# Kernel optimization log

Hardware: AMD Instinct MI355X
Metric: run time of the kernel (lower is better)

Reference implementation:

```python
import jax, jax.numpy as jnp
import numpy as np

N = 50000      # nodes
E = 800000     # edges (avg degree 16)
D = 128        # extended_lat_size = latent_size(124) + 4
G = 256        # number of graphs in the batch
H = 8 * D      # 1024, hidden width of MLP stack


def _w(k, shape):
    return jax.random.normal(k, shape, jnp.float32) * 0.02


def setup_inputs() -> dict:
    key = jax.random.key(0)
    ks = jax.random.split(key, 20)
    x = jax.random.normal(ks[0], (N, D), jnp.float32)
    edge_index = jax.random.randint(ks[1], (2, E), 0, N, dtype=jnp.int32)
    batch_vector = jnp.sort(jax.random.randint(ks[2], (N,), 0, G, dtype=jnp.int32))
    return {
        "x": x,
        "edge_index": edge_index,
        "batch_vector": batch_vector,
        # GCNConv layers
        "W1": _w(ks[3], (D, 2 * D)), "b1": jnp.zeros((2 * D,), jnp.float32),
        "W2": _w(ks[4], (2 * D, D)), "b2": jnp.zeros((D,), jnp.float32),
        # lazy Linear stack (in-dims resolved from dataflow)
        "Wl1": _w(ks[5], (D, D)),   "bl1": jnp.zeros((D,), jnp.float32),
        "Wl2": _w(ks[6], (D, H)),   "bl2": jnp.zeros((H,), jnp.float32),
        "Wl22": _w(ks[7], (H, H)),  "bl22": jnp.zeros((H,), jnp.float32),
        "Wl23": _w(ks[8], (H, H)),  "bl23": jnp.zeros((H,), jnp.float32),
        "Wl3": _w(ks[9], (H, D)),   "bl3": jnp.zeros((D,), jnp.float32),
    }


def gcn_conv(x, W, b, row, col):
    """PyG GCNConv: linear transform, add self-loops, symmetric norm, scatter-add."""
    h = x @ W  # [N, F_out]
    n = x.shape[0]
    loop = jnp.arange(n, dtype=row.dtype)
    r = jnp.concatenate([row, loop])   # source nodes
    c = jnp.concatenate([col, loop])   # target nodes
    deg = jax.ops.segment_sum(jnp.ones_like(c, dtype=h.dtype), c, num_segments=n)
    dinv = jnp.where(deg > 0, jax.lax.rsqrt(deg), 0.0)
    norm = dinv[r] * dinv[c]                         # [E+N]
    msg = h[r] * norm[:, None]                       # gather + scale
    out = jax.ops.segment_sum(msg, c, num_segments=n)  # scatter-add
    return out + b


def global_mean_pool(x, batch, num_graphs):
    s = jax.ops.segment_sum(x, batch, num_segments=num_graphs)
    cnt = jax.ops.segment_sum(jnp.ones((x.shape[0],), x.dtype), batch, num_segments=num_graphs)
    return s / jnp.maximum(cnt, 1.0)[:, None]


def reference(x, edge_index, batch_vector, W1, b1, W2, b2,
              Wl1, bl1, Wl2, bl2, Wl22, bl22, Wl23, bl23, Wl3, bl3):
    row, col = edge_index[0], edge_index[1]
    h = jax.nn.relu(gcn_conv(x, W1, b1, row, col))
    h = jax.nn.relu(gcn_conv(h, W2, b2, row, col))
    g = global_mean_pool(h, batch_vector, G)         # [G, D]
    g = jax.nn.relu(g @ Wl1 + bl1)
    g = jax.nn.relu(g @ Wl2 + bl2)
    g = jax.nn.relu(g @ Wl22 + bl22)
    g = jax.nn.relu(g @ Wl23 + bl23)
    g = g @ Wl3 + bl3                                 # [G, D]
    return jnp.squeeze(g).reshape(-1)                 # flatten -> [G*D]
```

## Files before the change

kernel.cpp:

```cpp
#include <hip/hip_runtime.h>


typedef __attribute__((ext_vector_type(8))) short bf16x8;
typedef __attribute__((ext_vector_type(8))) ushort u16x8;
typedef __attribute__((ext_vector_type(4))) float f32x4;

#define ADJ_STRIDE 64

__device__ __forceinline__ ushort f2bf(float f) {
    unsigned u = __float_as_uint(f);
    unsigned r = (u + 0x7FFFu + ((u >> 16) & 1u)) >> 16;
    return (ushort)r;
}
__device__ __forceinline__ float bf2f(ushort h) {
    return __uint_as_float(((unsigned)h) << 16);
}
__device__ __forceinline__ float bflo(unsigned u) {
    return __uint_as_float(u << 16);
}
__device__ __forceinline__ float bfhi(unsigned u) {
    return __uint_as_float(u & 0xffff0000u);
}
__device__ __forceinline__ float idinv(int d) {
    return rsqrtf((float)(d + 1));
}
__device__ __forceinline__ void gload16(const ushort* g, ushort* l) {
    __builtin_amdgcn_global_load_lds(
        (const __attribute__((address_space(1))) void*)g,
        (__attribute__((address_space(3))) void*)l, 16, 0, 0);
}

#define SWZ(r) (((r) >> 1) & 3)

struct PreArgs {
    const int* row;
    const int* col;
    int E, N;
    int* indeg;
    int* adjf;
    const float* W[7];
    ushort* Th[7];
    ushort* Tl[7];
    int K[7], Nn[7], off[8];
    const float* x;
    ushort* xb;
    int total8;
    int nFill, nT;
};

__global__ __launch_bounds__(256) void preproc_mega_kernel(PreArgs a) {
    __shared__ float sm[64][65];
    int bid = blockIdx.x;
    int tid = threadIdx.x;

    if (bid < a.nFill) {
        int r = bid & 7, chunk = bid >> 3;
        int lo = (int)(((long long)a.N * r) >> 3);
        int hi = (int)(((long long)a.N * (r + 1)) >> 3);
        int E4 = a.E >> 2;
#pragma unroll
        for (int v = 0; v < 2; ++v) {
            int i = chunk * 512 + v * 256 + tid;
            if (i < E4) {
                int c0 = __builtin_nontemporal_load(a.col + i * 4 + 0);
                int c1 = __builtin_nontemporal_load(a.col + i * 4 + 1);
                int c2 = __builtin_nontemporal_load(a.col + i * 4 + 2);
                int c3 = __builtin_nontemporal_load(a.col + i * 4 + 3);
                int r0 = __builtin_nontemporal_load(a.row + i * 4 + 0);
                int r1 = __builtin_nontemporal_load(a.row + i * 4 + 1);
                int r2 = __builtin_nontemporal_load(a.row + i * 4 + 2);
                int r3 = __builtin_nontemporal_load(a.row + i * 4 + 3);
                if (c0 >= lo && c0 < hi) {
                    int p = atomicAdd(&a.indeg[c0], 1);
                    if (p < ADJ_STRIDE) a.adjf[(c0 << 6) + p] = r0;
                }
                if (c1 >= lo && c1 < hi) {
                    int p = atomicAdd(&a.indeg[c1], 1);
                    if (p < ADJ_STRIDE) a.adjf[(c1 << 6) + p] = r1;
                }
                if (c2 >= lo && c2 < hi) {
                    int p = atomicAdd(&a.indeg[c2], 1);
                    if (p < ADJ_STRIDE) a.adjf[(c2 << 6) + p] = r2;
                }
                if (c3 >= lo && c3 < hi) {
                    int p = atomicAdd(&a.indeg[c3], 1);
                    if (p < ADJ_STRIDE) a.adjf[(c3 << 6) + p] = r3;
                }
            }
        }
        if (bid == 0 && tid < (a.E & 3)) {
            int e = (a.E & ~3) + tid;
            int c = a.col[e];
            int p = atomicAdd(&a.indeg[c], 1);
            if (p < ADJ_STRIDE) a.adjf[(c << 6) + p] = a.row[e];
        }
        return;
    }

    if (bid < a.nFill + a.nT) {
        int b = bid - a.nFill;
        int j = 0;
#pragma unroll
        for (int t = 1; t < 7; ++t) if (b >= a.off[t]) j = t;
        int local = b - a.off[j];
        int K = a.K[j], Nn = a.Nn[j];
        int kt = K >> 6;
        int k0 = (local % kt) * 64, n0 = (local / kt) * 64;
        const float* W = a.W[j];
        ushort* Th = a.Th[j];
        ushort* Tl = a.Tl[j];

        int r = tid >> 2, cq = tid & 3;
#pragma unroll
        for (int i = 0; i < 4; ++i) {
            float4 v = *(const float4*)(W + (size_t)(k0 + r) * Nn + n0 + cq * 16 + i * 4);
            sm[r][cq * 16 + i * 4 + 0] = v.x;
            sm[r][cq * 16 + i * 4 + 1] = v.y;
            sm[r][cq * 16 + i * 4 + 2] = v.z;
            sm[r][cq * 16 + i * 4 + 3] = v.w;
        }
        __syncthreads();
        int n = tid >> 2, kq = tid & 3;
        ushort h[16], l[16];
#pragma unroll
        for (int i = 0; i < 16; ++i) {
            float v = sm[kq * 16 + i][n];
            h[i] = f2bf(v);
            l[i] = f2bf(v - bf2f(h[i]));
        }
        size_t o = (size_t)(n0 + n) * K + k0 + kq * 16;
        *(u16x8*)(&Th[o]) = *(u16x8*)&h[0];
        *(u16x8*)(&Th[o + 8]) = *(u16x8*)&h[8];
        *(u16x8*)(&Tl[o]) = *(u16x8*)&l[0];
        *(u16x8*)(&Tl[o + 8]) = *(u16x8*)&l[8];
        return;
    }

    {
        int idx = (bid - a.nFill - a.nT) * 256 + tid;
        if (idx >= a.total8) return;
        const float4* xp = (const float4*)a.x;
        float4 v0 = xp[idx * 2], v1 = xp[idx * 2 + 1];
        ushort h[8] = {f2bf(v0.x), f2bf(v0.y), f2bf(v0.z), f2bf(v0.w),
                       f2bf(v1.x), f2bf(v1.y), f2bf(v1.z), f2bf(v1.w)};
        *(u16x8*)(a.xb + (size_t)idx * 8) = *(u16x8*)&h[0];
    }
}

template<int MODE>
__global__ void aggregate_bf16_kernel(const ushort* __restrict__ hsb,
                                      const int* __restrict__ indeg,
                                      const int* __restrict__ adjf,
                                      const float* __restrict__ bias,
                                      ushort* __restrict__ outh, ushort* __restrict__ outl,
                                      int N) {
    int wv = (blockIdx.x * blockDim.x + threadIdx.x) >> 6;
    int lane = threadIdx.x & 63;
    int half = lane >> 5, l32 = lane & 31;
    int node = wv * 2 + half;
    bool active = node < N;
    int nd = active ? node : N - 1;
    const uint2* base = (const uint2*)hsb;
    int degRaw = indeg[nd];
    float dself = idinv(degRaw);
    uint2 sa = base[(size_t)nd * 32 + l32];
    float sw = (MODE == 1) ? dself : 1.f;
    float ax = sw * bflo(sa.x), ay = sw * bfhi(sa.x);
    float az = sw * bflo(sa.y), aw = sw * bfhi(sa.y);
    int s = nd << 6;
    int deg = active ? min(degRaw, ADJ_STRIDE) : 0;
    int mx = max(deg, __shfl_xor(deg, 32));
    for (int j = 0; j < mx; j += 16) {
        int idx[16]; float wgt[16];
#pragma unroll
        for (int k = 0; k < 16; ++k) {
            int jj = j + k;
            bool valid = jj < deg;
            int ld = adjf[s + (valid ? jj : 0)];
            idx[k] = valid ? ld : 0;
            wgt[k] = valid ? 1.f : 0.f;
        }
        uint2 v[16];
#pragma unroll
        for (int k = 0; k < 16; ++k) v[k] = base[(size_t)idx[k] * 32 + l32];
        if (MODE == 1) {
#pragma unroll
            for (int k = 0; k < 16; ++k) wgt[k] *= idinv(indeg[idx[k]]);
        }
#pragma unroll
        for (int k = 0; k < 16; ++k) {
            ax = fmaf(wgt[k], bflo(v[k].x), ax);
            ay = fmaf(wgt[k], bfhi(v[k].x), ay);
            az = fmaf(wgt[k], bflo(v[k].y), az);
            aw = fmaf(wgt[k], bfhi(v[k].y), aw);
        }
    }
    if (!active) return;
    if (MODE == 0) {
        float4 b = ((const float4*)bias)[l32];
        ax = fmaxf(fmaf(ax, dself, b.x), 0.f);
        ay = fmaxf(fmaf(ay, dself, b.y), 0.f);
        az = fmaxf(fmaf(az, dself, b.z), 0.f);
        aw = fmaxf(fmaf(aw, dself, b.w), 0.f);
        ushort h0 = f2bf(ax), h1 = f2bf(ay), h2 = f2bf(az), h3 = f2bf(aw);
        uint2 hv = make_uint2((unsigned)h0 | ((unsigned)h1 << 16),
                              (unsigned)h2 | ((unsigned)h3 << 16));
        ((uint2*)outh)[(size_t)node * 32 + l32] = hv;
    } else {
        ax *= dself; ay *= dself; az *= dself; aw *= dself;
        ushort h0 = f2bf(ax), h1 = f2bf(ay), h2 = f2bf(az), h3 = f2bf(aw);
        uint2 hv = make_uint2((unsigned)h0 | ((unsigned)h1 << 16),
                              (unsigned)h2 | ((unsigned)h3 << 16));
        ushort l0 = f2bf(ax - bf2f(h0)), l1 = f2bf(ay - bf2f(h1));
        ushort l2 = f2bf(az - bf2f(h2)), l3 = f2bf(aw - bf2f(h3));
        uint2 lv = make_uint2((unsigned)l0 | ((unsigned)l1 << 16),
                              (unsigned)l2 | ((unsigned)l3 << 16));
        ((uint2*)outh)[(size_t)node * 32 + l32] = hv;
        ((uint2*)outl)[(size_t)node * 32 + l32] = lv;
    }
}

__global__ __launch_bounds__(512) void gcn_mid_kernel(
        const ushort* __restrict__ Ah, const ushort* __restrict__ Al,
        const ushort* __restrict__ B1h, const ushort* __restrict__ B1l,
        const ushort* __restrict__ B2h, const ushort* __restrict__ B2l,
        const float* __restrict__ bias1, const int* __restrict__ indeg,
        ushort* __restrict__ outb, int M) {
    __shared__ __align__(16) ushort t1f[2 * 128 * 256 + 2 * 128 * 32];
    const int tid = threadIdx.x;
    const int w = tid >> 6, lane = tid & 63;
    const int bm = blockIdx.x * 128;
    const int sq = lane >> 4, r16 = lane & 15;

    {
        const int wr = w >> 2, wc = w & 3;
        f32x4 acc1[4][4];
#pragma unroll
        for (int i = 0; i < 4; ++i)
#pragma unroll
            for (int j = 0; j < 4; ++j) acc1[i][j] = (f32x4)0.f;

        for (int kk = 0; kk < 128; kk += 32) {
            {
                int rowi = w * 16 + (lane >> 2);
                int u = lane & 3;
                int colk = kk + 8 * (u ^ SWZ(rowi));
                gload16(Ah + (size_t)(bm + rowi) * 128 + colk, t1f + w * 512);
                gload16(Al + (size_t)(bm + rowi) * 128 + colk, t1f + 4096 + w * 512);
            }
#pragma unroll
            for (int v = 0; v < 2; ++v) {
                int chunk = v * 8 + w;
                int rowi = chunk * 16 + (lane >> 2);
                int u = lane & 3;
                int colk = kk + 8 * (u ^ SWZ(rowi));
                gload16(B1h + (size_t)rowi * 128 + colk, t1f + 8192 + chunk * 512);
                gload16(B1l + (size_t)rowi * 128 + colk, t1f + 16384 + chunk * 512);
            }
            __syncthreads();

            bf16x8 ah[4], al[4], bh[4], bl[4];
#pragma unroll
            for (int f = 0; f < 4; ++f) {
                int ra = wr * 64 + f * 16 + r16;
                int oa = ra * 32 + 8 * (sq ^ SWZ(ra));
                ah[f] = *(const bf16x8*)(t1f + oa);
                al[f] = *(const bf16x8*)(t1f + 4096 + oa);
                int rb = wc * 64 + f * 16 + r16;
                int ob = rb * 32 + 8 * (sq ^ SWZ(rb));
                bh[f] = *(const bf16x8*)(t1f + 8192 + ob);
                bl[f] = *(const bf16x8*)(t1f + 16384 + ob);
            }
#pragma unroll
            for (int i = 0; i < 4; ++i)
#pragma unroll
                for (int j = 0; j < 4; ++j) {
                    acc1[i][j] = __builtin_amdgcn_mfma_f32_16x16x32_bf16(ah[i], bh[j], acc1[i][j], 0, 0, 0);
                    acc1[i][j] = __builtin_amdgcn_mfma_f32_16x16x32_bf16(ah[i], bl[j], acc1[i][j], 0, 0, 0);
                    acc1[i][j] = __builtin_amdgcn_mfma_f32_16x16x32_bf16(al[i], bh[j], acc1[i][j], 0, 0, 0);
                }
            __syncthreads();
        }

        const int q4 = lane >> 4;
#pragma unroll
        for (int j = 0; j < 4; ++j) {
            int col = wc * 64 + j * 16 + r16;
            float bv = bias1[col];
            int cslot = col >> 3, coff = col & 7;
#pragma unroll
            for (int i = 0; i < 4; ++i) {
                int rowb = wr * 64 + i * 16 + q4 * 4;
#pragma unroll
                for (int r = 0; r < 4; ++r) {
                    int rowt = rowb + r;
                    float v = fmaxf(acc1[i][j][r] + bv, 0.f);
                    ushort h = f2bf(v);
                    ushort lo = f2bf(v - bf2f(h));
                    int a = rowt * 256 + (((cslot ^ (rowt & 7)) << 3) + coff);
                    t1f[a] = h;
                    t1f[32768 + a] = lo;
                }
            }
        }
    }

    {
        const int wr2 = w >> 1, wc2 = w & 1;
        const int q4 = lane >> 4;
        f32x4 acc2[2][4];
#pragma unroll
        for (int i = 0; i < 2; ++i)
#pragma unroll
            for (int j = 0; j < 4; ++j) acc2[i][j] = (f32x4)0.f;

        for (int kk = 0; kk < 256; kk += 32) {
            {
                int rowi = w * 16 + (lane >> 2);
                int u = lane & 3;
                int colk = kk + 8 * (u ^ SWZ(rowi));
                gload16(B2h + (size_t)rowi * 256 + colk, t1f + 65536 + w * 512);
                gload16(B2l + (size_t)rowi * 256 + colk, t1f + 69632 + w * 512);
            }
            __syncthreads();

            bf16x8 a2h[2], a2l[2], b2h[4], b2l[4];
#pragma unroll
            for (int f = 0; f < 2; ++f) {
                int ra = wr2 * 32 + f * 16 + r16;
                int k0 = kk + sq * 8;
                int ao = ra * 256 + (((k0 >> 3) ^ (ra & 7)) << 3);
                a2h[f] = *(const bf16x8*)(t1f + ao);
                a2l[f] = *(const bf16x8*)(t1f + 32768 + ao);
            }
#pragma unroll
            for (int f = 0; f < 4; ++f) {
                int rb = wc2 * 64 + f * 16 + r16;
                int ob = rb * 32 + 8 * (sq ^ SWZ(rb));
                b2h[f] = *(const bf16x8*)(t1f + 65536 + ob);
                b2l[f] = *(const bf16x8*)(t1f + 69632 + ob);
            }
#pragma unroll
            for (int i = 0; i < 2; ++i)
#pragma unroll
                for (int j = 0; j < 4; ++j) {
                    acc2[i][j] = __builtin_amdgcn_mfma_f32_16x16x32_bf16(a2h[i], b2h[j], acc2[i][j], 0, 0, 0);
                    acc2[i][j] = __builtin_amdgcn_mfma_f32_16x16x32_bf16(a2h[i], b2l[j], acc2[i][j], 0, 0, 0);
                    acc2[i][j] = __builtin_amdgcn_mfma_f32_16x16x32_bf16(a2l[i], b2h[j], acc2[i][j], 0, 0, 0);
                }
            __syncthreads();
        }

#pragma unroll
        for (int i = 0; i < 2; ++i) {
            int row0 = bm + wr2 * 32 + i * 16 + q4 * 4;
            if (row0 >= M) continue;
#pragma unroll
            for (int j = 0; j < 4; ++j) {
                int col = wc2 * 64 + j * 16 + r16;
#pragma unroll
                for (int r = 0; r < 4; ++r) {
                    float dv = idinv(indeg[row0 + r]);
                    outb[(size_t)(row0 + r) * 128 + col] =
                        f2bf(acc2[i][j][r] * dv);
                }
            }
        }
    }
}

template<int BM, int BN, int EPI>
__global__ __launch_bounds__(256) void gemm_bf16x3_kernel(
        const ushort* __restrict__ Ah, const ushort* __restrict__ Al,
        const ushort* __restrict__ Bth, const ushort* __restrict__ Btl,
        const float* __restrict__ bias,
        float* __restrict__ Cf, ushort* __restrict__ Ch, ushort* __restrict__ Cl,
        int M, int N, int K, int kChunk) {
    constexpr int WMm = BM / 2, WMn = BN / 2;
    constexpr int FRm = WMm / 16, FRn = WMn / 16;
    __shared__ __align__(16) ushort lds[(2 * BM + 2 * BN) * 32];
    const int tbB[4] = {0, BM * 64, 2 * BM * 64, (2 * BM + BN) * 64};

    const int tid = threadIdx.x;
    const int w = tid >> 6, lane = tid & 63;
    const int wr = w >> 1, wc = w & 1;
    const int bm = blockIdx.x * BM, bn = blockIdx.y * BN;
    const int k0 = blockIdx.z * kChunk;
    int k1 = k0 + kChunk; if (k1 > K) k1 = K;

    const ushort* srcs[4] = {
        Ah  + (size_t)bm * K, Al  + (size_t)bm * K,
        Bth + (size_t)bn * K, Btl + (size_t)bn * K };

    f32x4 acc[FRm][FRn];
#pragma unroll
    for (int i = 0; i < FRm; ++i)
#pragma unroll
        for (int j = 0; j < FRn; ++j) acc[i][j] = (f32x4)0.f;

    const int sq = lane >> 4, r16 = lane & 15;

    for (int kk = k0; kk < k1; kk += 32) {
#pragma unroll
        for (int t = 0; t < 4; ++t) {
            const int rows = (t < 2) ? BM : BN;
            const int nv = rows / 64;
#pragma unroll
            for (int v = 0; v < nv; ++v) {
                int chunk = v * 4 + w;
                int rowi = chunk * 16 + (lane >> 2);
                int u = lane & 3;
                int colk = kk + 8 * (u ^ SWZ(rowi));
                const ushort* g = srcs[t] + (size_t)rowi * K + colk;
                ushort* lp = (ushort*)((char*)lds + tbB[t] + chunk * 16 * 64);
                gload16(g, lp);
            }
        }
        __syncthreads();

        bf16x8 ah[FRm], al[FRm], bh[FRn], bl[FRn];
#pragma unroll
        for (int f = 0; f < FRm; ++f) {
            int ra = wr * WMm + f * 16 + r16;
            int oa = ra * 64 + 16 * (sq ^ SWZ(ra));
            ah[f] = *(const bf16x8*)((const char*)lds + tbB[0] + oa);
            al[f] = *(const bf16x8*)((const char*)lds + tbB[1] + oa);
        }
#pragma unroll
        for (int f = 0; f < FRn; ++f) {
            int rb = wc * WMn + f * 16 + r16;
            int ob = rb * 64 + 16 * (sq ^ SWZ(rb));
            bh[f] = *(const bf16x8*)((const char*)lds + tbB[2] + ob);
            bl[f] = *(const bf16x8*)((const char*)lds + tbB[3] + ob);
        }

#pragma unroll
        for (int i = 0; i < FRm; ++i)
#pragma unroll
            for (int j = 0; j < FRn; ++j) {
                acc[i][j] = __builtin_amdgcn_mfma_f32_16x16x32_bf16(ah[i], bh[j], acc[i][j], 0, 0, 0);
                acc[i][j] = __builtin_amdgcn_mfma_f32_16x16x32_bf16(ah[i], bl[j], acc[i][j], 0, 0, 0);
                acc[i][j] = __builtin_amdgcn_mfma_f32_16x16x32_bf16(al[i], bh[j], acc[i][j], 0, 0, 0);
            }
        __syncthreads();
    }

    const int q4 = lane >> 4;
#pragma unroll
    for (int i = 0; i < FRm; ++i) {
        int row0 = bm + wr * WMm + i * 16 + q4 * 4;
        if (row0 >= M) continue;
#pragma unroll
        for (int j = 0; j < FRn; ++j) {
            int colc = bn + wc * WMn + j * 16 + r16;
            if (EPI == 1) {
                float bv = bias[colc];
#pragma unroll
                for (int r = 0; r < 4; ++r) {
                    float v = fmaxf(acc[i][j][r] + bv, 0.f);
                    ushort h = f2bf(v);
                    ushort lo = f2bf(v - bf2f(h));
                    size_t o = (size_t)(row0 + r) * N + colc;
                    Ch[o] = h; Cl[o] = lo;
                }
            } else {
#pragma unroll
                for (int r = 0; r < 4; ++r)
                    atomicAdd(&Cf[(size_t)(row0 + r) * N + colc], acc[i][j][r]);
            }
        }
    }
}

__global__ void finish_kernel(const float* __restrict__ acc, const float* __restrict__ bias,
                              float* __restrict__ outf, ushort* __restrict__ outh,
                              ushort* __restrict__ outl, int total, int Ncols, int doRelu) {
    int idx = blockIdx.x * blockDim.x + threadIdx.x;
    if (idx >= total) return;
    float v = acc[idx] + bias[idx & (Ncols - 1)];
    if (doRelu) v = fmaxf(v, 0.f);
    if (outh) {
        ushort h = f2bf(v);
        outh[idx] = h;
        outl[idx] = f2bf(v - bf2f(h));
    } else {
        outf[idx] = v;
    }
}

__global__ void pool_kernel(const ushort* __restrict__ feats, const int* __restrict__ batch,
                            ushort* __restrict__ gh, ushort* __restrict__ gl, int N) {
    __shared__ float sm[256];
    int gid = blockIdx.x;
    int lo = 0, hi = N;
    while (lo < hi) { int m = (lo + hi) >> 1; if (batch[m] < gid) lo = m + 1; else hi = m; }
    int start = lo;
    lo = start; hi = N;
    while (lo < hi) { int m = (lo + hi) >> 1; if (batch[m] < gid + 1) lo = m + 1; else hi = m; }
    int end = lo;
    int tid = threadIdx.x;
    int f = tid & 127, half = tid >> 7;
    float acc = 0.f;
    for (int i = start + half; i < end; i += 2) acc += bf2f(feats[(size_t)i * 128 + f]);
    sm[tid] = acc;
    __syncthreads();
    if (half == 0) {
        acc += sm[tid + 128];
        int cnt = end - start; if (cnt < 1) cnt = 1;
        float m = acc / (float)cnt;
        ushort h = f2bf(m);
        gh[gid * 128 + f] = h;
        gl[gid * 128 + f] = f2bf(m - bf2f(h));
    }
}


extern "C" void kernel_launch(void* const* d_in, const int* in_sizes, int n_in,
                              void* d_out, int out_size, void* d_ws, size_t ws_size,
                              hipStream_t stream) {
    const float* x    = (const float*)d_in[0];
    const int*   ei   = (const int*)d_in[1];
    const int*   batch= (const int*)d_in[2];
    const float* W1   = (const float*)d_in[3];
    const float* b1   = (const float*)d_in[4];
    const float* W2   = (const float*)d_in[5];
    const float* b2   = (const float*)d_in[6];
    const float* Wl1  = (const float*)d_in[7];
    const float* bl1  = (const float*)d_in[8];
    const float* Wl2  = (const float*)d_in[9];
    const float* bl2  = (const float*)d_in[10];
    const float* Wl22 = (const float*)d_in[11];
    const float* bl22 = (const float*)d_in[12];
    const float* Wl23 = (const float*)d_in[13];
    const float* bl23 = (const float*)d_in[14];
    const float* Wl3  = (const float*)d_in[15];
    const float* bl3  = (const float*)d_in[16];

    const int D = 128;
    const int N = in_sizes[0] / D;
    const int E = in_sizes[1] / 2;
    const int G = out_size / D;
    const int H = in_sizes[10];
    const int Mpad = ((N + 127) / 128) * 128;
    const int* row = ei;
    const int* col = ei + E;
    float* out = (float*)d_out;

    char* ws = (char*)d_ws;
    auto alloc = [&](size_t bytes) -> void* {
        void* p = (void*)ws;
        ws += (bytes + 255) & ~(size_t)255;
        return p;
    };
    int*    indeg  = (int*)alloc((size_t)N * 4);
    float*  accb   = (float*)alloc((size_t)G * H * 4);
    float*  accb2  = (float*)alloc((size_t)G * H * 4);
    float*  accf   = (float*)alloc((size_t)G * 128 * 4);
    char*   zeroEnd = ws;
    int*    adjf   = (int*)alloc((size_t)N * ADJ_STRIDE * 4);
    ushort* W1th   = (ushort*)alloc((size_t)256 * 128 * 2);
    ushort* W1tl   = (ushort*)alloc((size_t)256 * 128 * 2);
    ushort* W2th   = (ushort*)alloc((size_t)128 * 256 * 2);
    ushort* W2tl   = (ushort*)alloc((size_t)128 * 256 * 2);
    ushort* Tl1h  = (ushort*)alloc((size_t)128 * 128 * 2);
    ushort* Tl1l  = (ushort*)alloc((size_t)128 * 128 * 2);
    ushort* Tl2h  = (ushort*)alloc((size_t)H * 128 * 2);
    ushort* Tl2l  = (ushort*)alloc((size_t)H * 128 * 2);
    ushort* Tl22h = (ushort*)alloc((size_t)H * H * 2);
    ushort* Tl22l = (ushort*)alloc((size_t)H * H * 2);
    ushort* Tl23h = (ushort*)alloc((size_t)H * H * 2);
    ushort* Tl23l = (ushort*)alloc((size_t)H * H * 2);
    ushort* Tl3h  = (ushort*)alloc((size_t)128 * H * 2);
    ushort* Tl3l  = (ushort*)alloc((size_t)128 * H * 2);
    ushort* xb     = (ushort*)alloc((size_t)Mpad * 128 * 2);
    ushort* yh     = (ushort*)alloc((size_t)Mpad * 128 * 2);
    ushort* yl     = (ushort*)alloc((size_t)Mpad * 128 * 2);
    ushort* hs2b   = (ushort*)alloc((size_t)Mpad * 128 * 2);
    ushort* yfb    = (ushort*)alloc((size_t)Mpad * 128 * 2);
    ushort* gh     = (ushort*)alloc((size_t)G * 128 * 2);
    ushort* gl     = (ushort*)alloc((size_t)G * 128 * 2);
    ushort* a1h    = (ushort*)alloc((size_t)G * 128 * 2);
    ushort* a1l    = (ushort*)alloc((size_t)G * 128 * 2);
    ushort* a2h    = (ushort*)alloc((size_t)G * H * 2);
    ushort* a2l    = (ushort*)alloc((size_t)G * H * 2);
    ushort* a3h    = (ushort*)alloc((size_t)G * H * 2);
    ushort* a3l    = (ushort*)alloc((size_t)G * H * 2);
    ushort* a4h    = (ushort*)alloc((size_t)G * H * 2);
    ushort* a4l    = (ushort*)alloc((size_t)G * H * 2);

    hipMemsetAsync(indeg, 0, (size_t)(zeroEnd - (char*)indeg), stream);

    const int CHUNKS = (E / 4 + 511) / 512;
    {
        PreArgs pa;
        pa.row = row; pa.col = col; pa.E = E; pa.N = N;
        pa.indeg = indeg; pa.adjf = adjf;
        const float* Ws[7]  = {W1, W2, Wl1, Wl2, Wl22, Wl23, Wl3};
        ushort* Ths[7]      = {W1th, W2th, Tl1h, Tl2h, Tl22h, Tl23h, Tl3h};
        ushort* Tls[7]      = {W1tl, W2tl, Tl1l, Tl2l, Tl22l, Tl23l, Tl3l};
        int Ks[7]           = {128, 256, 128, 128, H, H, H};
        int Nns[7]          = {256, 128, 128, H, H, H, 128};
        int off = 0;
        for (int j = 0; j < 7; ++j) {
            pa.W[j] = Ws[j]; pa.Th[j] = Ths[j]; pa.Tl[j] = Tls[j];
            pa.K[j] = Ks[j]; pa.Nn[j] = Nns[j];
            pa.off[j] = off;
            off += (Ks[j] / 64) * (Nns[j] / 64);
        }
        pa.off[7] = off;
        pa.x = x; pa.xb = xb; pa.total8 = N * 16;
        pa.nFill = 8 * CHUNKS;
        pa.nT = off;
        int nCvt = (pa.total8 + 255) / 256;
        preproc_mega_kernel<<<pa.nFill + pa.nT + nCvt, 256, 0, stream>>>(pa);
    }

    aggregate_bf16_kernel<1><<<(N + 7) / 8, 256, 0, stream>>>(
        xb, indeg, adjf, nullptr, yh, yl, N);

    gcn_mid_kernel<<<Mpad / 128, 512, 0, stream>>>(
        yh, yl, W1th, W1tl, W2th, W2tl, b1, indeg, hs2b, N);

    aggregate_bf16_kernel<0><<<(N + 7) / 8, 256, 0, stream>>>(
        hs2b, indeg, adjf, b2, yfb, nullptr, N);

    pool_kernel<<<G, 256, 0, stream>>>(yfb, batch, gh, gl, N);

    {
        dim3 grid(G / 64, 2);
        gemm_bf16x3_kernel<64, 64, 1><<<grid, 256, 0, stream>>>(
            gh, gl, Tl1h, Tl1l, bl1, nullptr, a1h, a1l, G, 128, 128, 128);
    }
    {
        dim3 grid(G / 64, H / 64);
        gemm_bf16x3_kernel<64, 64, 1><<<grid, 256, 0, stream>>>(
            a1h, a1l, Tl2h, Tl2l, bl2, nullptr, a2h, a2l, G, H, 128, 128);
    }
    {
        dim3 grid(G / 64, H / 64, 8);
        gemm_bf16x3_kernel<64, 64, 3><<<grid, 256, 0, stream>>>(
            a2h, a2l, Tl22h, Tl22l, nullptr, accb, nullptr, nullptr, G, H, H, 128);
        finish_kernel<<<(G * H + 255) / 256, 256, 0, stream>>>(
            accb, bl22, nullptr, a3h, a3l, G * H, H, 1);
    }
    {
        dim3 grid(G / 64, H / 64, 8);
        gemm_bf16x3_kernel<64, 64, 3><<<grid, 256, 0, stream>>>(
            a3h, a3l, Tl23h, Tl23l, nullptr, accb2, nullptr, nullptr, G, H, H, 128);
        finish_kernel<<<(G * H + 255) / 256, 256, 0, stream>>>(
            accb2, bl23, nullptr, a4h, a4l, G * H, H, 1);
    }
    {
        dim3 grid(G / 64, 2, 8);
        gemm_bf16x3_kernel<64, 64, 3><<<grid, 256, 0, stream>>>(
            a4h, a4l, Tl3h, Tl3l, nullptr, accf, nullptr, nullptr, G, 128, H, 128);
        finish_kernel<<<(G * 128 + 255) / 256, 256, 0, stream>>>(
            accf, bl3, out, nullptr, nullptr, G * 128, 128, 0);
    }
}
```

Baseline: 242.4 us.

## Widen aggregation gathers to 16B, prescale source features, vectorize adjacency loads

```diff
diff --git a/kernel.cpp b/kernel.cpp
--- a/kernel.cpp
+++ b/kernel.cpp
@@ -147,6 +147,18 @@
     }
 }
 
+__global__ void scale_xb_kernel(ushort* __restrict__ xb, const int* __restrict__ indeg,
+                                int total8) {
+    int idx = blockIdx.x * blockDim.x + threadIdx.x;
+    if (idx >= total8) return;
+    float dv = idinv(indeg[idx >> 4]);
+    u16x8 v = *(u16x8*)(xb + (size_t)idx * 8);
+    ushort h[8];
+#pragma unroll
+    for (int i = 0; i < 8; ++i) h[i] = f2bf(dv * bf2f((ushort)v[i]));
+    *(u16x8*)(xb + (size_t)idx * 8) = *(u16x8*)&h[0];
+}
+
 template<int MODE>
 __global__ void aggregate_bf16_kernel(const ushort* __restrict__ hsb,
                                       const int* __restrict__ indeg,
@@ -156,67 +168,83 @@
                                       int N) {
     int wv = (blockIdx.x * blockDim.x + threadIdx.x) >> 6;
     int lane = threadIdx.x & 63;
-    int half = lane >> 5, l32 = lane & 31;
-    int node = wv * 2 + half;
+    int grp = lane >> 4, l16 = lane & 15;
+    int node = wv * 4 + grp;
     bool active = node < N;
     int nd = active ? node : N - 1;
-    const uint2* base = (const uint2*)hsb;
+    const uint4* base = (const uint4*)hsb;
     int degRaw = indeg[nd];
     float dself = idinv(degRaw);
-    uint2 sa = base[(size_t)nd * 32 + l32];
-    float sw = (MODE == 1) ? dself : 1.f;
-    float ax = sw * bflo(sa.x), ay = sw * bfhi(sa.x);
-    float az = sw * bflo(sa.y), aw = sw * bfhi(sa.y);
+    uint4 sa = base[(size_t)nd * 16 + l16];
+    float a0 = bflo(sa.x), a1 = bfhi(sa.x), a2 = bflo(sa.y), a3 = bfhi(sa.y);
+    float a4 = bflo(sa.z), a5 = bfhi(sa.z), a6 = bflo(sa.w), a7 = bfhi(sa.w);
     int s = nd << 6;
     int deg = active ? min(degRaw, ADJ_STRIDE) : 0;
-    int mx = max(deg, __shfl_xor(deg, 32));
-    for (int j = 0; j < mx; j += 16) {
-        int idx[16]; float wgt[16];
-#pragma unroll
-        for (int k = 0; k < 16; ++k) {
-            int jj = j + k;
-            bool valid = jj < deg;
-            int ld = adjf[s + (valid ? jj : 0)];
-            idx[k] = valid ? ld : 0;
+    int mx = deg;
+    mx = max(mx, __shfl_xor(mx, 16));
+    mx = max(mx, __shfl_xor(mx, 32));
+    for (int j = 0; j < mx; j += 8) {
+        int4 q0 = *(const int4*)(adjf + s + j);
+        int4 q1 = *(const int4*)(adjf + s + j + 4);
+        int idx[8]; float wgt[8];
+        idx[0] = q0.x; idx[1] = q0.y; idx[2] = q0.z; idx[3] = q0.w;
+        idx[4] = q1.x; idx[5] = q1.y; idx[6] = q1.z; idx[7] = q1.w;
+#pragma unroll
+        for (int k = 0; k < 8; ++k) {
+            bool valid = (j + k) < deg;
+            idx[k] = valid ? idx[k] : 0;
             wgt[k] = valid ? 1.f : 0.f;
         }
-        uint2 v[16];
-#pragma unroll
-        for (int k = 0; k < 16; ++k) v[k] = base[(size_t)idx[k] * 32 + l32];
-        if (MODE == 1) {
-#pragma unroll
-            for (int k = 0; k < 16; ++k) wgt[k] *= idinv(indeg[idx[k]]);
-        }
-#pragma unroll
-        for (int k = 0; k < 16; ++k) {
-            ax = fmaf(wgt[k], bflo(v[k].x), ax);
-            ay = fmaf(wgt[k], bfhi(v[k].x), ay);
-            az = fmaf(wgt[k], bflo(v[k].y), az);
-            aw = fmaf(wgt[k], bfhi(v[k].y), aw);
+        uint4 v[8];
+#pragma unroll
+        for (int k = 0; k < 8; ++k) v[k] = base[(size_t)idx[k] * 16 + l16];
+#pragma unroll
+        for (int k = 0; k < 8; ++k) {
+            a0 = fmaf(wgt[k], bflo(v[k].x), a0);
+            a1 = fmaf(wgt[k], bfhi(v[k].x), a1);
+            a2 = fmaf(wgt[k], bflo(v[k].y), a2);
+            a3 = fmaf(wgt[k], bfhi(v[k].y), a3);
+            a4 = fmaf(wgt[k], bflo(v[k].z), a4);
+            a5 = fmaf(wgt[k], bfhi(v[k].z), a5);
+            a6 = fmaf(wgt[k], bflo(v[k].w), a6);
+            a7 = fmaf(wgt[k], bfhi(v[k].w), a7);
         }
     }
     if (!active) return;
     if (MODE == 0) {
-        float4 b = ((const float4*)bias)[l32];
-        ax = fmaxf(fmaf(ax, dself, b.x), 0.f);
-        ay = fmaxf(fmaf(ay, dself, b.y), 0.f);
-        az = fmaxf(fmaf(az, dself, b.z), 0.f);
-        aw = fmaxf(fmaf(aw, dself, b.w), 0.f);
-        ushort h0 = f2bf(ax), h1 = f2bf(ay), h2 = f2bf(az), h3 = f2bf(aw);
-        uint2 hv = make_uint2((unsigned)h0 | ((unsigned)h1 << 16),
-                              (unsigned)h2 | ((unsigned)h3 << 16));
-        ((uint2*)outh)[(size_t)node * 32 + l32] = hv;
+        float4 b0 = *(const float4*)(bias + l16 * 8);
+        float4 b1 = *(const float4*)(bias + l16 * 8 + 4);
+        a0 = fmaxf(fmaf(a0, dself, b0.x), 0.f);
+        a1 = fmaxf(fmaf(a1, dself, b0.y), 0.f);
+        a2 = fmaxf(fmaf(a2, dself, b0.z), 0.f);
+        a3 = fmaxf(fmaf(a3, dself, b0.w), 0.f);
+        a4 = fmaxf(fmaf(a4, dself, b1.x), 0.f);
+        a5 = fmaxf(fmaf(a5, dself, b1.y), 0.f);
+        a6 = fmaxf(fmaf(a6, dself, b1.z), 0.f);
+        a7 = fmaxf(fmaf(a7, dself, b1.w), 0.f);
+        uint4 hv;
+        hv.x = (unsigned)f2bf(a0) | ((unsigned)f2bf(a1) << 16);
+        hv.y = (unsigned)f2bf(a2) | ((unsigned)f2bf(a3) << 16);
+        hv.z = (unsigned)f2bf(a4) | ((unsigned)f2bf(a5) << 16);
+        hv.w = (unsigned)f2bf(a6) | ((unsigned)f2bf(a7) << 16);
+        ((uint4*)outh)[(size_t)node * 16 + l16] = hv;
     } else {
-        ax *= dself; ay *= dself; az *= dself; aw *= dself;
-        ushort h0 = f2bf(ax), h1 = f2bf(ay), h2 = f2bf(az), h3 = f2bf(aw);
-        uint2 hv = make_uint2((unsigned)h0 | ((unsigned)h1 << 16),
-                              (unsigned)h2 | ((unsigned)h3 << 16));
-        ushort l0 = f2bf(ax - bf2f(h0)), l1 = f2bf(ay - bf2f(h1));
-        ushort l2 = f2bf(az - bf2f(h2)), l3 = f2bf(aw - bf2f(h3));
-        uint2 lv = make_uint2((unsigned)l0 | ((unsigned)l1 << 16),
-                              (unsigned)l2 | ((unsigned)l3 << 16));
-        ((uint2*)outh)[(size_t)node * 32 + l32] = hv;
-        ((uint2*)outl)[(size_t)node * 32 + l32] = lv;
+        a0 *= dself; a1 *= dself; a2 *= dself; a3 *= dself;
+        a4 *= dself; a5 *= dself; a6 *= dself; a7 *= dself;
+        ushort h0 = f2bf(a0), h1 = f2bf(a1), h2 = f2bf(a2), h3 = f2bf(a3);
+        ushort h4 = f2bf(a4), h5 = f2bf(a5), h6 = f2bf(a6), h7 = f2bf(a7);
+        uint4 hv;
+        hv.x = (unsigned)h0 | ((unsigned)h1 << 16);
+        hv.y = (unsigned)h2 | ((unsigned)h3 << 16);
+        hv.z = (unsigned)h4 | ((unsigned)h5 << 16);
+        hv.w = (unsigned)h6 | ((unsigned)h7 << 16);
+        uint4 lv;
+        lv.x = (unsigned)f2bf(a0 - bf2f(h0)) | ((unsigned)f2bf(a1 - bf2f(h1)) << 16);
+        lv.y = (unsigned)f2bf(a2 - bf2f(h2)) | ((unsigned)f2bf(a3 - bf2f(h3)) << 16);
+        lv.z = (unsigned)f2bf(a4 - bf2f(h4)) | ((unsigned)f2bf(a5 - bf2f(h5)) << 16);
+        lv.w = (unsigned)f2bf(a6 - bf2f(h6)) | ((unsigned)f2bf(a7 - bf2f(h7)) << 16);
+        ((uint4*)outh)[(size_t)node * 16 + l16] = hv;
+        ((uint4*)outl)[(size_t)node * 16 + l16] = lv;
     }
 }
 
@@ -615,13 +643,15 @@
         preproc_mega_kernel<<<pa.nFill + pa.nT + nCvt, 256, 0, stream>>>(pa);
     }
 
-    aggregate_bf16_kernel<1><<<(N + 7) / 8, 256, 0, stream>>>(
+    scale_xb_kernel<<<(N * 16 + 255) / 256, 256, 0, stream>>>(xb, indeg, N * 16);
+
+    aggregate_bf16_kernel<1><<<(N + 15) / 16, 256, 0, stream>>>(
         xb, indeg, adjf, nullptr, yh, yl, N);
 
     gcn_mid_kernel<<<Mpad / 128, 512, 0, stream>>>(
         yh, yl, W1th, W1tl, W2th, W2tl, b1, indeg, hs2b, N);
 
-    aggregate_bf16_kernel<0><<<(N + 7) / 8, 256, 0, stream>>>(
+    aggregate_bf16_kernel<0><<<(N + 15) / 16, 256, 0, stream>>>(
         hs2b, indeg, adjf, b2, yfb, nullptr, N);
 
     pool_kernel<<<G, 256, 0, stream>>>(yfb, batch, gh, gl, N);
```

Result: faster. 235.7 us (-2.7%).
